# Kernel tuning notes

Measured on AMD Instinct MI355X. Metric: run time of the kernel, lower is better.

The kernel has to match this reference:

```python
import jax, jax.numpy as jnp
import numpy as np

EMBED_DIM = 1024
NUM_HEADS = 16
MICRO_HEADS = 8
HEAD_DIM = EMBED_DIM // NUM_HEADS
N_BLOCKS = NUM_HEADS // MICRO_HEADS
B, N = 2, 2048


def setup_inputs() -> dict:
    key = jax.random.key(0)
    ks = jax.random.split(key, 9)
    s = 1.0 / np.sqrt(EMBED_DIM)
    return {
        "x": jax.random.normal(ks[0], (B, N, EMBED_DIM), dtype=jnp.float32),
        "Wq": jax.random.uniform(ks[1], (EMBED_DIM, EMBED_DIM), jnp.float32, -s, s),
        "bq": jax.random.uniform(ks[2], (EMBED_DIM,), jnp.float32, -s, s),
        "Wk": jax.random.uniform(ks[3], (EMBED_DIM, EMBED_DIM), jnp.float32, -s, s),
        "bk": jax.random.uniform(ks[4], (EMBED_DIM,), jnp.float32, -s, s),
        "Wv": jax.random.uniform(ks[5], (EMBED_DIM, EMBED_DIM), jnp.float32, -s, s),
        "bv": jax.random.uniform(ks[6], (EMBED_DIM,), jnp.float32, -s, s),
        "Wo": jax.random.uniform(ks[7], (EMBED_DIM, EMBED_DIM), jnp.float32, -s, s),
        "bo": jax.random.uniform(ks[8], (EMBED_DIM,), jnp.float32, -s, s),
    }


def _scramble(t, b, n):
    # Replicates torch's Qh[:, :, hs:he, :].contiguous().view(B*mh, N, dh)
    # which is a raw row-major reshape mixing (N, mh) -> (mh, N) per batch.
    # (B, N, E) -> (B, N, nb, mh, dh) -> (B, nb, N, mh, dh) -> raw reshape -> (B, nb, mh, N, dh)
    t = t.reshape(b, n, N_BLOCKS, MICRO_HEADS, HEAD_DIM)
    t = jnp.transpose(t, (0, 2, 1, 3, 4))
    return t.reshape(b, N_BLOCKS, MICRO_HEADS, n, HEAD_DIM)


def reference(x, Wq, bq, Wk, bk, Wv, bv, Wo, bo):
    b, n, e = x.shape
    scale = HEAD_DIM ** -0.5
    Q = x @ Wq.T + bq
    K = x @ Wk.T + bk
    V = x @ Wv.T + bv
    q = _scramble(Q, b, n)  # (B, nb, mh, N, dh)
    k = _scramble(K, b, n)
    v = _scramble(V, b, n)
    s = jnp.einsum("bgmqd,bgmkd->bgmqk", q, k) * scale  # (B, nb, mh, N, N)
    causal = jnp.tril(jnp.ones((n, n), dtype=bool))
    s = jnp.where(causal, s, -jnp.inf)
    p = jax.nn.softmax(s, axis=-1)
    ctx = jnp.einsum("bgmqk,bgmkd->bgmqd", p, v)  # (B, nb, mh, N, dh)
    # inverse raw reshape: (mh, N, dh) -> (N, mh*dh) per (b, g), then concat blocks
    ctx = ctx.reshape(b, N_BLOCKS, n, MICRO_HEADS * HEAD_DIM)
    ctx = jnp.transpose(ctx, (0, 2, 1, 3)).reshape(b, n, e)
    return ctx @ Wo.T + bo
```

## Files before the change

### kernel.cpp

```cpp
#include <hip/hip_runtime.h>
#include <hip/hip_bf16.h>


typedef unsigned short ushortT;
typedef __attribute__((ext_vector_type(8))) short short8;
typedef __attribute__((ext_vector_type(4))) float floatx4;
typedef __attribute__((ext_vector_type(2))) unsigned int uintx2;

__device__ inline void gl_lds16(const ushortT* g, ushortT* lds) {
    __builtin_amdgcn_global_load_lds(
        (const __attribute__((address_space(1))) unsigned int*)g,
        (__attribute__((address_space(3))) unsigned int*)lds, 16, 0, 0);
}

__global__ __launch_bounds__(256) void cvt_bf16(
    const float* __restrict__ x,
    const float* __restrict__ Wq, const float* __restrict__ Wk,
    const float* __restrict__ Wv, const float* __restrict__ Wo,
    ushortT* __restrict__ xb, ushortT* __restrict__ Wb)
{
    const unsigned tid = blockIdx.x * 256 + threadIdx.x;
    const size_t e = (size_t)tid * 8;
    const float* src;
    ushortT* dst;
    size_t off;
    if (e < (size_t)(4u << 20)) { src = x; dst = xb; off = e; }
    else {
        const size_t r = e - (size_t)(4u << 20);
        const int wsel = (int)(r >> 20);
        off = r & 0xFFFFFu;
        src = (wsel == 0) ? Wq : (wsel == 1) ? Wk : (wsel == 2) ? Wv : Wo;
        dst = Wb + ((size_t)wsel << 20);
    }
    const float4 f0 = ((const float4*)(src + off))[0];
    const float4 f1 = ((const float4*)(src + off))[1];
    union { __hip_bfloat162 h[4]; uint4 u; } pk;
    pk.h[0] = __float22bfloat162_rn(float2{f0.x, f0.y});
    pk.h[1] = __float22bfloat162_rn(float2{f0.z, f0.w});
    pk.h[2] = __float22bfloat162_rn(float2{f1.x, f1.y});
    pk.h[3] = __float22bfloat162_rn(float2{f1.z, f1.w});
    *(uint4*)(dst + off) = pk.u;
}

__global__ __launch_bounds__(512, 2) void gemm_qkv_8p(
    const ushortT* __restrict__ A, const ushortT* __restrict__ Wst,
    const float* __restrict__ b0, const float* __restrict__ b1, const float* __restrict__ b2,
    ushortT* __restrict__ O0, ushortT* __restrict__ O1, ushortT* __restrict__ O2)
{
    __shared__ __align__(16) ushortT sm[65536];

    const int t = threadIdx.x;
    const int bid = blockIdx.x;
    const int wg = (bid & 7) * 24 + (bid >> 3);
    const int mt = wg / 12;
    const int nt = wg - mt * 12;
    const int m0 = mt * 256;
    const int mat = nt >> 2;
    const int n0 = (nt & 3) * 256;
    const ushortT* W = Wst + ((size_t)mat << 20);
    const float* bias = (mat == 0) ? b0 : (mat == 1) ? b1 : b2;
    ushortT* Out     = (mat == 0) ? O0 : (mat == 1) ? O1 : O2;
    const float oscale = (mat == 0) ? 0.18033688f : 1.0f;

    const int w = t >> 6, lane = t & 63;
    const int wm = w >> 2, wn = w & 3;
    const int col16 = lane & 15, quad = lane >> 4;
    const int c7 = col16 & 7;

    const int ko[2] = { ((0 + quad) ^ c7) << 3, ((4 + quad) ^ c7) << 3 };
    const int xbase = (wm * 128 + col16) * 64;
    const int wbase = (wn * 64 + col16) * 64;

    const int trow = t >> 3;
    const int sch = (t & 7) ^ (trow & 7);
    const ushortT* gA[4]; const ushortT* gB[4];
    #pragma unroll
    for (int q = 0; q < 4; q++) {
        gA[q] = A + (size_t)(m0 + q * 64 + trow) * 1024 + sch * 8;
        gB[q] = W + (size_t)(n0 + q * 64 + trow) * 1024 + sch * 8;
    }
    const int dst0 = (w << 6) * 8;

    floatx4 acc[8][4];
    #pragma unroll
    for (int i = 0; i < 8; i++)
        #pragma unroll
        for (int j = 0; j < 4; j++) acc[i][j] = (floatx4)0.0f;

    auto issue8 = [&](const int ab, const int bb) {
        #pragma unroll
        for (int q = 0; q < 4; q++) {
            gl_lds16(gA[q], sm + ab + dst0 + q * 4096);
            gl_lds16(gB[q], sm + bb + dst0 + q * 4096);
            gA[q] += 64; gB[q] += 64;
        }
    };

    auto group = [&](const int ab, const int bb) {
        short8 bw[4];
        #pragma unroll
        for (int ks = 0; ks < 2; ks++) {
            #pragma unroll
            for (int mh = 0; mh < 2; mh++) {
                short8 bx[4];
                if (mh == 0) {
                    #pragma unroll
                    for (int nf = 0; nf < 4; nf++)
                        bw[nf] = *(const short8*)(sm + bb + wbase + nf * 1024 + ko[ks]);
                }
                #pragma unroll
                for (int j = 0; j < 4; j++)
                    bx[j] = *(const short8*)(sm + ab + xbase + (mh * 4 + j) * 1024 + ko[ks]);
                __builtin_amdgcn_s_barrier();
                __builtin_amdgcn_s_setprio(1);
                #pragma unroll
                for (int j = 0; j < 4; j++)
                    #pragma unroll
                    for (int nf = 0; nf < 4; nf++)
                        acc[mh * 4 + j][nf] = __builtin_amdgcn_mfma_f32_16x16x32_bf16(
                            bw[nf], bx[j], acc[mh * 4 + j][nf], 0, 0, 0);
                __builtin_amdgcn_s_setprio(0);
                __builtin_amdgcn_s_barrier();
            }
        }
    };

    issue8(0, 16384);
    issue8(32768, 49152);

    #pragma unroll 1
    for (int it = 0; it < 7; ++it) {
        asm volatile("s_waitcnt vmcnt(8)" ::: "memory");
        __builtin_amdgcn_s_barrier();
        group(0, 16384);
        issue8(0, 16384);
        asm volatile("s_waitcnt vmcnt(8)" ::: "memory");
        __builtin_amdgcn_s_barrier();
        group(32768, 49152);
        issue8(32768, 49152);
    }
    asm volatile("s_waitcnt vmcnt(8)" ::: "memory");
    __builtin_amdgcn_s_barrier();
    group(0, 16384);
    asm volatile("s_waitcnt vmcnt(0)" ::: "memory");
    __builtin_amdgcn_s_barrier();
    group(32768, 49152);

    #pragma unroll
    for (int mf = 0; mf < 8; mf++) {
        const int m = m0 + wm * 128 + mf * 16 + col16;
        #pragma unroll
        for (int nf = 0; nf < 4; nf++) {
            const int nb = n0 + wn * 64 + nf * 16 + quad * 4;
            const float4 bv4 = *(const float4*)(bias + nb);
            const float v0 = (acc[mf][nf][0] + bv4.x) * oscale;
            const float v1 = (acc[mf][nf][1] + bv4.y) * oscale;
            const float v2 = (acc[mf][nf][2] + bv4.z) * oscale;
            const float v3 = (acc[mf][nf][3] + bv4.w) * oscale;
            union { __hip_bfloat162 h[2]; unsigned long long u; } pk2;
            pk2.h[0] = __float22bfloat162_rn(float2{v0, v1});
            pk2.h[1] = __float22bfloat162_rn(float2{v2, v3});
            *(unsigned long long*)(Out + (size_t)m * 1024 + nb) = pk2.u;
        }
    }
}

template <bool OUT_F32, bool N64>
__global__ __launch_bounds__(256) void gemm_lds(
    const ushortT* __restrict__ A, const ushortT* __restrict__ Wst,
    const float* __restrict__ b0, const float* __restrict__ b1, const float* __restrict__ b2,
    void* __restrict__ O0, void* __restrict__ O1, void* __restrict__ O2)
{
    constexpr int NT = N64 ? 64 : 128;
    constexpr int NJ = N64 ? 2 : 4;
    constexpr int WQ = N64 ? 2 : 4;
    __shared__ __align__(16) ushortT As[128 * 64];
    __shared__ __align__(16) ushortT Bs[NT * 64];
    const int t = threadIdx.x;
    const int m0 = blockIdx.y * 128;
    const int n0g = blockIdx.x * NT;
    const int mat = n0g >> 10;
    const int n0 = n0g & 1023;
    const ushortT* W = Wst + ((size_t)mat << 20);
    const float* bias = (mat == 0) ? b0 : (mat == 1) ? b1 : b2;
    void* Out        = (mat == 0) ? O0 : (mat == 1) ? O1 : O2;

    const int w = t >> 6, lane = t & 63;
    const int wm = w >> 1, wn = w & 1;
    const int col16 = lane & 15, quad = lane >> 4;

    floatx4 acc[4][NJ];
    for (int i = 0; i < 4; i++)
        for (int j = 0; j < NJ; j++) acc[i][j] = (floatx4)0.0f;

    const int cid0 = w * (N64 ? 128 : 256) + lane;

    for (int k0 = 0; k0 < 1024; k0 += 64) {
        #pragma unroll
        for (int q = 0; q < 4; q++) {
            const int cid = w * 256 + q * 64 + lane;
            const int row = cid >> 3;
            const int sch = (cid & 7) ^ (row & 7);
            gl_lds16(A + (size_t)(m0 + row) * 1024 + k0 + sch * 8,
                     As + (size_t)(w * 256 + q * 64) * 8);
        }
        #pragma unroll
        for (int q = 0; q < WQ; q++) {
            const int cid = cid0 + q * 64;
            const int row = cid >> 3;
            const int sch = (cid & 7) ^ (row & 7);
            gl_lds16(W + (size_t)(n0 + row) * 1024 + k0 + sch * 8,
                     Bs + (size_t)(w * (N64 ? 128 : 256) + q * 64) * 8);
        }
        __syncthreads();
        #pragma unroll
        for (int ks = 0; ks < 64; ks += 32) {
            const int cbase = (ks >> 3) + quad;
            const int sw = col16 & 7;
            short8 a[4], b[NJ];
            #pragma unroll
            for (int i = 0; i < 4; i++) {
                const int row = wm * 64 + i * 16 + col16;
                a[i] = *(const short8*)(As + row * 64 + ((cbase ^ sw) << 3));
            }
            #pragma unroll
            for (int j = 0; j < NJ; j++) {
                const int row = wn * (NT / 2) + j * 16 + col16;
                b[j] = *(const short8*)(Bs + row * 64 + ((cbase ^ sw) << 3));
            }
            #pragma unroll
            for (int i = 0; i < 4; i++)
                #pragma unroll
                for (int j = 0; j < NJ; j++)
                    acc[i][j] = __builtin_amdgcn_mfma_f32_16x16x32_bf16(b[j], a[i], acc[i][j], 0, 0, 0);
        }
        __syncthreads();
    }

    #pragma unroll
    for (int i = 0; i < 4; i++) {
        const int m = m0 + wm * 64 + i * 16 + col16;
        #pragma unroll
        for (int j = 0; j < NJ; j++) {
            const int nb = n0 + wn * (NT / 2) + j * 16 + quad * 4;
            const float4 bv4 = *(const float4*)(bias + nb);
            const float v0 = acc[i][j][0] + bv4.x;
            const float v1 = acc[i][j][1] + bv4.y;
            const float v2 = acc[i][j][2] + bv4.z;
            const float v3 = acc[i][j][3] + bv4.w;
            if constexpr (OUT_F32) {
                *(float4*)((float*)Out + (size_t)m * 1024 + nb) = float4{v0, v1, v2, v3};
            } else {
                union { __hip_bfloat162 h[2]; unsigned long long u; } pk2;
                pk2.h[0] = __float22bfloat162_rn(float2{v0, v1});
                pk2.h[1] = __float22bfloat162_rn(float2{v2, v3});
                *(unsigned long long*)((ushortT*)Out + (size_t)m * 1024 + nb) = pk2.u;
            }
        }
    }
}

__global__ __launch_bounds__(256) void transpose_v(
    const ushortT* __restrict__ Vb, ushortT* __restrict__ VT)
{
    __shared__ ushortT L[64 * 65];
    const int bid = blockIdx.x;
    const int pt = bid & 31, s = bid >> 5;
    const int bb = s >> 4, g = (s >> 3) & 1, mh = s & 7;
    const size_t baseoff = (size_t)bb * 2048 * 1024 + (size_t)g * 512;
    const int t = threadIdx.x;
    {
        const int pr = t >> 2, seg = t & 3;
        const int i = mh * 2048 + pt * 64 + pr;
        const uint4* src = (const uint4*)(Vb + baseoff + (size_t)(i >> 3) * 1024 + (i & 7) * 64 + seg * 16);
        union { uint4 u[2]; ushortT h[16]; } tmp;
        tmp.u[0] = src[0]; tmp.u[1] = src[1];
        #pragma unroll
        for (int d = 0; d < 16; d++) L[pr * 65 + seg * 16 + d] = tmp.h[d];
    }
    __syncthreads();
    {
        const int dc = t >> 2, pseg = t & 3;
        union { uint4 u[2]; ushortT h[16]; } tmp;
        #pragma unroll
        for (int j = 0; j < 16; j++) tmp.h[j] = L[(pseg * 16 + j) * 65 + dc];
        uint4* dst = (uint4*)(VT + (size_t)s * 64 * 2048 + (size_t)dc * 2048 + pt * 64 + pseg * 16);
        dst[0] = tmp.u[0]; dst[1] = tmp.u[1];
    }
}

__global__ __launch_bounds__(256) void attn(
    const ushortT* __restrict__ Qb, const ushortT* __restrict__ Kb,
    const ushortT* __restrict__ VT, ushortT* __restrict__ Cb)
{
    __shared__ __align__(16) ushortT lds[16384];

    const int t = threadIdx.x;
    const int bid = blockIdx.x;
    const int xcd = bid & 7;
    const int u = bid >> 3;
    const int s = xcd * 4 + (u & 3);
    const int x5 = u >> 2;
    const int qt = (x5 < 8) ? x5 : (x5 < 16) ? (39 - x5)
                 : (x5 < 24) ? (x5 - 8) : (47 - x5);
    const int bb = s >> 4, g = (s >> 3) & 1, mh = s & 7;

    const int w = t >> 6, lane = t & 63;
    const int col16 = lane & 15, quad = lane >> 4;

    const size_t baseoff = (size_t)bb * 2048 * 1024 + (size_t)g * 512;
    const size_t vtbase  = (size_t)s * 64 * 2048;
    const int i0 = mh * 2048 + qt * 64;
    const int qloc = w * 16 + col16;
    const int c7 = col16 & 7;

    short8 qreg[2];
    {
        const int i = i0 + qloc;
        const ushortT* p = Qb + baseoff + (size_t)(i >> 3) * 1024 + (i & 7) * 64;
        qreg[0] = *(const short8*)(p + quad * 8);
        qreg[1] = *(const short8*)(p + 32 + quad * 8);
    }

    int kbo[2];
    kbo[0] = col16 * 64 + (((0 + quad) ^ c7) << 3);
    kbo[1] = col16 * 64 + (((4 + quad) ^ c7) << 3);

    const int cid0 = w * 128 + lane, cid1 = cid0 + 64;
    const int row0 = cid0 >> 3, sch0 = (cid0 & 7) ^ (row0 & 7);
    const int row1 = cid1 >> 3, sch1 = (cid1 & 7) ^ (row1 & 7);
    const int jr0 = mh * 2048 + row0;
    const int jr1 = mh * 2048 + row1;
    const ushortT* gk0 = Kb + baseoff + (size_t)(jr0 >> 3) * 1024 + (jr0 & 7) * 64 + sch0 * 8;
    const ushortT* gk1 = Kb + baseoff + (size_t)(jr1 >> 3) * 1024 + (jr1 & 7) * 64 + sch1 * 8;
    const ushortT* gv0 = VT + vtbase + (size_t)row0 * 2048 + sch0 * 8;
    const ushortT* gv1 = VT + vtbase + (size_t)row1 * 2048 + sch1 * 8;
    const int sdK = w * 1024;

    auto stage = [&](int sb) {
        gl_lds16(gk0, lds + sb + sdK);
        gl_lds16(gk1, lds + sb + sdK + 512);
        gl_lds16(gv0, lds + sb + 8192 + sdK);
        gl_lds16(gv1, lds + sb + 8192 + sdK + 512);
        gk0 += 8192; gk1 += 8192; gv0 += 64; gv1 += 64;
    };

    float l4[4] = {0.f, 0.f, 0.f, 0.f};
    floatx4 Oacc[4];
    for (int c = 0; c < 4; c++) Oacc[c] = (floatx4)0.0f;

    stage(0);
    int sb = 4096;
    for (int kt = 0; kt <= qt; ++kt) {
        __syncthreads();
        if (kt < qt) { stage(sb); sb ^= 4096; }

        floatx4 sc[4];
        for (int c = 0; c < 4; c++) sc[c] = (floatx4)0.0f;
        #pragma unroll
        for (int h = 0; h < 2; h++) {
            const short8 bq = qreg[h];
            #pragma unroll
            for (int c = 0; c < 4; c++) {
                const short8 ak = *(const short8*)(lds + kbo[h] + c * 1024);
                sc[c] = __builtin_amdgcn_mfma_f32_16x16x32_bf16(ak, bq, sc[c], 0, 0, 0);
            }
        }

        if (kt == qt) {
            #pragma unroll
            for (int c = 0; c < 4; c++)
                #pragma unroll
                for (int r = 0; r < 4; r++)
                    if ((c * 16 + quad * 4 + r) > qloc) sc[c][r] = -1e30f;
        }

        unsigned pw[4][2];
        #pragma unroll
        for (int c = 0; c < 4; c++) {
            float pv0 = __builtin_amdgcn_exp2f(sc[c][0]);
            float pv1 = __builtin_amdgcn_exp2f(sc[c][1]);
            float pv2 = __builtin_amdgcn_exp2f(sc[c][2]);
            float pv3 = __builtin_amdgcn_exp2f(sc[c][3]);
            l4[0] += pv0; l4[1] += pv1; l4[2] += pv2; l4[3] += pv3;
            union { __hip_bfloat162 h; unsigned u; } a, b;
            a.h = __float22bfloat162_rn(float2{pv0, pv1});
            b.h = __float22bfloat162_rn(float2{pv2, pv3});
            pw[c][0] = a.u; pw[c][1] = b.u;
        }

        #pragma unroll
        for (int h = 0; h < 2; h++) {
            unsigned dw[4];
            #pragma unroll
            for (int uu = 0; uu < 2; uu++) {
                uintx2 s32 = __builtin_amdgcn_permlane32_swap(pw[2 * h][uu], pw[2 * h + 1][uu], false, false);
                uintx2 s16 = __builtin_amdgcn_permlane16_swap(s32.x, s32.y, false, false);
                dw[uu] = s16.x; dw[2 + uu] = s16.y;
            }
            union { unsigned u[4]; short8 s; } bpu;
            bpu.u[0] = dw[0]; bpu.u[1] = dw[1]; bpu.u[2] = dw[2]; bpu.u[3] = dw[3];
            const short8 bp = bpu.s;
            #pragma unroll
            for (int c = 0; c < 4; c++) {
                const short8 av = *(const short8*)(lds + kbo[h] + 8192 + c * 1024);
                Oacc[c] = __builtin_amdgcn_mfma_f32_16x16x32_bf16(av, bp, Oacc[c], 0, 0, 0);
            }
        }

        kbo[0] ^= 4096; kbo[1] ^= 4096;
    }

    float l_s = (l4[0] + l4[1]) + (l4[2] + l4[3]);
    l_s += __shfl_xor(l_s, 16);
    l_s += __shfl_xor(l_s, 32);

    {
        const int i = i0 + qloc;
        const float inv = 1.0f / l_s;
        ushortT* dst = Cb + baseoff + (size_t)(i >> 3) * 1024 + (i & 7) * 64;
        #pragma unroll
        for (int c = 0; c < 4; c++) {
            union { __hip_bfloat162 h[2]; unsigned long long u; } pk2;
            pk2.h[0] = __float22bfloat162_rn(float2{Oacc[c][0] * inv, Oacc[c][1] * inv});
            pk2.h[1] = __float22bfloat162_rn(float2{Oacc[c][2] * inv, Oacc[c][3] * inv});
            *(unsigned long long*)(dst + c * 16 + quad * 4) = pk2.u;
        }
    }
}

extern "C" void kernel_launch(void* const* d_in, const int* in_sizes, int n_in,
                              void* d_out, int out_size, void* d_ws, size_t ws_size,
                              hipStream_t stream)
{
    const float* x  = (const float*)d_in[0];
    const float* Wq = (const float*)d_in[1];
    const float* bq = (const float*)d_in[2];
    const float* Wk = (const float*)d_in[3];
    const float* bk = (const float*)d_in[4];
    const float* Wv = (const float*)d_in[5];
    const float* bv = (const float*)d_in[6];
    const float* Wo = (const float*)d_in[7];
    const float* bo = (const float*)d_in[8];

    const size_t M1 = (size_t)1024 * 1024;
    ushortT* Wb  = (ushortT*)d_ws;
    ushortT* xb  = Wb + 4 * M1;
    ushortT* Qb  = xb + 4 * M1;
    ushortT* Kb  = Qb + 4 * M1;
    ushortT* Vb  = (ushortT*)d_out;
    ushortT* VTb = xb;
    ushortT* Cb  = Qb;

    dim3 blk(256);
    cvt_bf16<<<dim3(4096), blk, 0, stream>>>(x, Wq, Wk, Wv, Wo, xb, Wb);
    gemm_qkv_8p<<<dim3(192), dim3(512), 0, stream>>>(
        xb, Wb, bq, bk, bv, Qb, Kb, Vb);
    transpose_v<<<dim3(1024), blk, 0, stream>>>(Vb, VTb);
    attn<<<dim3(1024), blk, 0, stream>>>(Qb, Kb, VTb, Cb);
    gemm_lds<true, true><<<dim3(16, 32), blk, 0, stream>>>(
        Cb, Wb + 3 * M1, bo, bo, bo, d_out, d_out, d_out);
}
```

Measured before the change: 184.0 us.

## Double query tile per attention block to reuse K/V LDS tiles

Each attention block now handles 128 query rows instead of 64, with each wave owning two 16-row query fragments that share the same K and V LDS reads. The grid halves to 512 blocks and the causal tile schedule is remapped to pair tiles for load balance. This cuts K/V global loads and LDS reads per query, at the cost of more registers per thread (doubled accumulators and scores), fewer blocks in flight, and extra masked work on the diagonal tiles.

```diff
diff --git a/kernel.cpp b/kernel.cpp
--- a/kernel.cpp
+++ b/kernel.cpp
@@ -300,9 +300,8 @@
     const int xcd = bid & 7;
     const int u = bid >> 3;
     const int s = xcd * 4 + (u & 3);
-    const int x5 = u >> 2;
-    const int qt = (x5 < 8) ? x5 : (x5 < 16) ? (39 - x5)
-                 : (x5 < 24) ? (x5 - 8) : (47 - x5);
+    const int x4 = u >> 2;
+    const int p = (x4 < 8) ? x4 : 23 - x4;
     const int bb = s >> 4, g = (s >> 3) & 1, mh = s & 7;
 
     const int w = t >> 6, lane = t & 63;
@@ -310,16 +309,19 @@
 
     const size_t baseoff = (size_t)bb * 2048 * 1024 + (size_t)g * 512;
     const size_t vtbase  = (size_t)s * 64 * 2048;
-    const int i0 = mh * 2048 + qt * 64;
-    const int qloc = w * 16 + col16;
+    const int i0 = mh * 2048 + p * 128;
+    const int ntile = 2 * p + 2;
     const int c7 = col16 & 7;
 
-    short8 qreg[2];
-    {
-        const int i = i0 + qloc;
-        const ushortT* p = Qb + baseoff + (size_t)(i >> 3) * 1024 + (i & 7) * 64;
-        qreg[0] = *(const short8*)(p + quad * 8);
-        qreg[1] = *(const short8*)(p + 32 + quad * 8);
+    const int qloc[2] = { w * 32 + col16, w * 32 + 16 + col16 };
+
+    short8 qreg[2][2];
+    #pragma unroll
+    for (int qf = 0; qf < 2; qf++) {
+        const int i = i0 + qloc[qf];
+        const ushortT* ptr = Qb + baseoff + (size_t)(i >> 3) * 1024 + (i & 7) * 64;
+        qreg[qf][0] = *(const short8*)(ptr + quad * 8);
+        qreg[qf][1] = *(const short8*)(ptr + 32 + quad * 8);
     }
 
     int kbo[2];
@@ -345,85 +347,111 @@
         gk0 += 8192; gk1 += 8192; gv0 += 64; gv1 += 64;
     };
 
-    float l4[4] = {0.f, 0.f, 0.f, 0.f};
-    floatx4 Oacc[4];
-    for (int c = 0; c < 4; c++) Oacc[c] = (floatx4)0.0f;
+    float l4[2][4];
+    floatx4 Oacc[2][4];
+    #pragma unroll
+    for (int qf = 0; qf < 2; qf++)
+        #pragma unroll
+        for (int c = 0; c < 4; c++) { Oacc[qf][c] = (floatx4)0.0f; l4[qf][c] = 0.f; }
 
     stage(0);
     int sb = 4096;
-    for (int kt = 0; kt <= qt; ++kt) {
+    #pragma unroll 1
+    for (int kt = 0; kt < ntile; ++kt) {
         __syncthreads();
-        if (kt < qt) { stage(sb); sb ^= 4096; }
-
-        floatx4 sc[4];
-        for (int c = 0; c < 4; c++) sc[c] = (floatx4)0.0f;
+        if (kt < ntile - 1) { stage(sb); sb ^= 4096; }
+
+        floatx4 sc[2][4];
+        #pragma unroll
+        for (int qf = 0; qf < 2; qf++)
+            #pragma unroll
+            for (int c = 0; c < 4; c++) sc[qf][c] = (floatx4)0.0f;
         #pragma unroll
         for (int h = 0; h < 2; h++) {
-            const short8 bq = qreg[h];
+            short8 ak[4];
+            #pragma unroll
+            for (int c = 0; c < 4; c++)
+                ak[c] = *(const short8*)(lds + kbo[h] + c * 1024);
+            #pragma unroll
+            for (int qf = 0; qf < 2; qf++)
+                #pragma unroll
+                for (int c = 0; c < 4; c++)
+                    sc[qf][c] = __builtin_amdgcn_mfma_f32_16x16x32_bf16(
+                        ak[c], qreg[qf][h], sc[qf][c], 0, 0, 0);
+        }
+
+        const int dk = kt - 2 * p;
+        if (dk >= 0) {
+            #pragma unroll
+            for (int qf = 0; qf < 2; qf++) {
+                const int qe = qloc[qf] - 64 * dk;
+                #pragma unroll
+                for (int c = 0; c < 4; c++)
+                    #pragma unroll
+                    for (int r = 0; r < 4; r++)
+                        if ((c * 16 + quad * 4 + r) > qe) sc[qf][c][r] = -1e30f;
+            }
+        }
+
+        unsigned pw[2][4][2];
+        #pragma unroll
+        for (int qf = 0; qf < 2; qf++)
             #pragma unroll
             for (int c = 0; c < 4; c++) {
-                const short8 ak = *(const short8*)(lds + kbo[h] + c * 1024);
-                sc[c] = __builtin_amdgcn_mfma_f32_16x16x32_bf16(ak, bq, sc[c], 0, 0, 0);
-            }
-        }
-
-        if (kt == qt) {
+                float pv0 = __builtin_amdgcn_exp2f(sc[qf][c][0]);
+                float pv1 = __builtin_amdgcn_exp2f(sc[qf][c][1]);
+                float pv2 = __builtin_amdgcn_exp2f(sc[qf][c][2]);
+                float pv3 = __builtin_amdgcn_exp2f(sc[qf][c][3]);
+                l4[qf][0] += pv0; l4[qf][1] += pv1;
+                l4[qf][2] += pv2; l4[qf][3] += pv3;
+                union { __hip_bfloat162 h; unsigned u; } a, b;
+                a.h = __float22bfloat162_rn(float2{pv0, pv1});
+                b.h = __float22bfloat162_rn(float2{pv2, pv3});
+                pw[qf][c][0] = a.u; pw[qf][c][1] = b.u;
+            }
+
+        #pragma unroll
+        for (int h = 0; h < 2; h++) {
+            short8 av[4];
             #pragma unroll
             for (int c = 0; c < 4; c++)
-                #pragma unroll
-                for (int r = 0; r < 4; r++)
-                    if ((c * 16 + quad * 4 + r) > qloc) sc[c][r] = -1e30f;
-        }
-
-        unsigned pw[4][2];
-        #pragma unroll
-        for (int c = 0; c < 4; c++) {
-            float pv0 = __builtin_amdgcn_exp2f(sc[c][0]);
-            float pv1 = __builtin_amdgcn_exp2f(sc[c][1]);
-            float pv2 = __builtin_amdgcn_exp2f(sc[c][2]);
-            float pv3 = __builtin_amdgcn_exp2f(sc[c][3]);
-            l4[0] += pv0; l4[1] += pv1; l4[2] += pv2; l4[3] += pv3;
-            union { __hip_bfloat162 h; unsigned u; } a, b;
-            a.h = __float22bfloat162_rn(float2{pv0, pv1});
-            b.h = __float22bfloat162_rn(float2{pv2, pv3});
-            pw[c][0] = a.u; pw[c][1] = b.u;
-        }
-
-        #pragma unroll
-        for (int h = 0; h < 2; h++) {
-            unsigned dw[4];
-            #pragma unroll
-            for (int uu = 0; uu < 2; uu++) {
-                uintx2 s32 = __builtin_amdgcn_permlane32_swap(pw[2 * h][uu], pw[2 * h + 1][uu], false, false);
-                uintx2 s16 = __builtin_amdgcn_permlane16_swap(s32.x, s32.y, false, false);
-                dw[uu] = s16.x; dw[2 + uu] = s16.y;
-            }
-            union { unsigned u[4]; short8 s; } bpu;
-            bpu.u[0] = dw[0]; bpu.u[1] = dw[1]; bpu.u[2] = dw[2]; bpu.u[3] = dw[3];
-            const short8 bp = bpu.s;
-            #pragma unroll
-            for (int c = 0; c < 4; c++) {
-                const short8 av = *(const short8*)(lds + kbo[h] + 8192 + c * 1024);
-                Oacc[c] = __builtin_amdgcn_mfma_f32_16x16x32_bf16(av, bp, Oacc[c], 0, 0, 0);
+                av[c] = *(const short8*)(lds + kbo[h] + 8192 + c * 1024);
+            #pragma unroll
+            for (int qf = 0; qf < 2; qf++) {
+                unsigned dw[4];
+                #pragma unroll
+                for (int uu = 0; uu < 2; uu++) {
+                    uintx2 s32 = __builtin_amdgcn_permlane32_swap(
+                        pw[qf][2 * h][uu], pw[qf][2 * h + 1][uu], false, false);
+                    uintx2 s16 = __builtin_amdgcn_permlane16_swap(s32.x, s32.y, false, false);
+                    dw[uu] = s16.x; dw[2 + uu] = s16.y;
+                }
+                union { unsigned u[4]; short8 s; } bpu;
+                bpu.u[0] = dw[0]; bpu.u[1] = dw[1]; bpu.u[2] = dw[2]; bpu.u[3] = dw[3];
+                const short8 bp = bpu.s;
+                #pragma unroll
+                for (int c = 0; c < 4; c++)
+                    Oacc[qf][c] = __builtin_amdgcn_mfma_f32_16x16x32_bf16(
+                        av[c], bp, Oacc[qf][c], 0, 0, 0);
             }
         }
 
         kbo[0] ^= 4096; kbo[1] ^= 4096;
     }
 
-    float l_s = (l4[0] + l4[1]) + (l4[2] + l4[3]);
-    l_s += __shfl_xor(l_s, 16);
-    l_s += __shfl_xor(l_s, 32);
-
-    {
-        const int i = i0 + qloc;
+    #pragma unroll
+    for (int qf = 0; qf < 2; qf++) {
+        float l_s = (l4[qf][0] + l4[qf][1]) + (l4[qf][2] + l4[qf][3]);
+        l_s += __shfl_xor(l_s, 16);
+        l_s += __shfl_xor(l_s, 32);
         const float inv = 1.0f / l_s;
+        const int i = i0 + qloc[qf];
         ushortT* dst = Cb + baseoff + (size_t)(i >> 3) * 1024 + (i & 7) * 64;
         #pragma unroll
         for (int c = 0; c < 4; c++) {
             union { __hip_bfloat162 h[2]; unsigned long long u; } pk2;
-            pk2.h[0] = __float22bfloat162_rn(float2{Oacc[c][0] * inv, Oacc[c][1] * inv});
-            pk2.h[1] = __float22bfloat162_rn(float2{Oacc[c][2] * inv, Oacc[c][3] * inv});
+            pk2.h[0] = __float22bfloat162_rn(float2{Oacc[qf][c][0] * inv, Oacc[qf][c][1] * inv});
+            pk2.h[1] = __float22bfloat162_rn(float2{Oacc[qf][c][2] * inv, Oacc[qf][c][3] * inv});
             *(unsigned long long*)(dst + c * 16 + quad * 4) = pk2.u;
         }
     }
@@ -457,7 +485,7 @@
     gemm_qkv_8p<<<dim3(192), dim3(512), 0, stream>>>(
         xb, Wb, bq, bk, bv, Qb, Kb, Vb);
     transpose_v<<<dim3(1024), blk, 0, stream>>>(Vb, VTb);
-    attn<<<dim3(1024), blk, 0, stream>>>(Qb, Kb, VTb, Cb);
+    attn<<<dim3(512), blk, 0, stream>>>(Qb, Kb, VTb, Cb);
     gemm_lds<true, true><<<dim3(16, 32), blk, 0, stream>>>(
         Cb, Wb + 3 * M1, bo, bo, bo, d_out, d_out, d_out);
 }
```

Result: slower. 189.0 us (+2.8%).

## Switch attention to 32x32x16 MFMA with two-wave blocks of 32 query rows

Applied to the files above, without the earlier changes.

Rewrites the attention kernel to use 32x32x16 bf16 MFMA tiles instead of 16x16x32, with 128-thread blocks where each wave handles 32 query rows of the 64-row tile. The P-matrix repacking uses only permlane32 swaps, the causal mask and output layout are remapped for the 32x32 accumulator layout, and s_setprio is raised around the MFMA bursts. The intent is fewer MFMA issues, fewer LDS reads per FLOP and less shuffle overhead. The trade-off is more registers per wave and half as many waves per block, which may lower occupancy and latency hiding.

```diff
diff --git a/kernel.cpp b/kernel.cpp
--- a/kernel.cpp
+++ b/kernel.cpp
@@ -5,6 +5,7 @@
 typedef unsigned short ushortT;
 typedef __attribute__((ext_vector_type(8))) short short8;
 typedef __attribute__((ext_vector_type(4))) float floatx4;
+typedef __attribute__((ext_vector_type(16))) float floatx16;
 typedef __attribute__((ext_vector_type(2))) unsigned int uintx2;
 
 __device__ inline void gl_lds16(const ushortT* g, ushortT* lds) {
@@ -289,7 +290,7 @@
     }
 }
 
-__global__ __launch_bounds__(256) void attn(
+__global__ __launch_bounds__(128) void attn(
     const ushortT* __restrict__ Qb, const ushortT* __restrict__ Kb,
     const ushortT* __restrict__ VT, ushortT* __restrict__ Cb)
 {
@@ -306,126 +307,142 @@
     const int bb = s >> 4, g = (s >> 3) & 1, mh = s & 7;
 
     const int w = t >> 6, lane = t & 63;
-    const int col16 = lane & 15, quad = lane >> 4;
+    const int l31 = lane & 31, h = lane >> 5;
 
     const size_t baseoff = (size_t)bb * 2048 * 1024 + (size_t)g * 512;
     const size_t vtbase  = (size_t)s * 64 * 2048;
     const int i0 = mh * 2048 + qt * 64;
-    const int qloc = w * 16 + col16;
-    const int c7 = col16 & 7;
-
-    short8 qreg[2];
+    const int qloc = w * 32 + l31;
+
+    short8 qreg[4];
     {
         const int i = i0 + qloc;
         const ushortT* p = Qb + baseoff + (size_t)(i >> 3) * 1024 + (i & 7) * 64;
-        qreg[0] = *(const short8*)(p + quad * 8);
-        qreg[1] = *(const short8*)(p + 32 + quad * 8);
-    }
-
-    int kbo[2];
-    kbo[0] = col16 * 64 + (((0 + quad) ^ c7) << 3);
-    kbo[1] = col16 * 64 + (((4 + quad) ^ c7) << 3);
-
-    const int cid0 = w * 128 + lane, cid1 = cid0 + 64;
-    const int row0 = cid0 >> 3, sch0 = (cid0 & 7) ^ (row0 & 7);
-    const int row1 = cid1 >> 3, sch1 = (cid1 & 7) ^ (row1 & 7);
-    const int jr0 = mh * 2048 + row0;
-    const int jr1 = mh * 2048 + row1;
-    const ushortT* gk0 = Kb + baseoff + (size_t)(jr0 >> 3) * 1024 + (jr0 & 7) * 64 + sch0 * 8;
-    const ushortT* gk1 = Kb + baseoff + (size_t)(jr1 >> 3) * 1024 + (jr1 & 7) * 64 + sch1 * 8;
-    const ushortT* gv0 = VT + vtbase + (size_t)row0 * 2048 + sch0 * 8;
-    const ushortT* gv1 = VT + vtbase + (size_t)row1 * 2048 + sch1 * 8;
-    const int sdK = w * 1024;
-
-    auto stage = [&](int sb) {
-        gl_lds16(gk0, lds + sb + sdK);
-        gl_lds16(gk1, lds + sb + sdK + 512);
-        gl_lds16(gv0, lds + sb + 8192 + sdK);
-        gl_lds16(gv1, lds + sb + 8192 + sdK + 512);
-        gk0 += 8192; gk1 += 8192; gv0 += 64; gv1 += 64;
+        #pragma unroll
+        for (int dc = 0; dc < 4; dc++)
+            qreg[dc] = *(const short8*)(p + dc * 16 + h * 8);
+    }
+
+    int off[2][4];
+    #pragma unroll
+    for (int a = 0; a < 2; a++)
+        #pragma unroll
+        for (int b = 0; b < 4; b++)
+            off[a][b] = (a * 32 + l31) * 64 + ((((b << 1) + h) ^ (lane & 7)) << 3);
+
+    const ushortT* gk[4]; const ushortT* gv[4];
+    int ldk[4];
+    #pragma unroll
+    for (int j = 0; j < 4; j++) {
+        const int cid = j * 128 + t;
+        const int row = cid >> 3;
+        const int sch = (cid & 7) ^ (row & 7);
+        const int jr = mh * 2048 + row;
+        gk[j] = Kb + baseoff + (size_t)(jr >> 3) * 1024 + (jr & 7) * 64 + sch * 8;
+        gv[j] = VT + vtbase + (size_t)row * 2048 + sch * 8;
+        ldk[j] = j * 1024 + w * 512;
+    }
+
+    auto stage = [&](int sbw) {
+        #pragma unroll
+        for (int j = 0; j < 4; j++) {
+            gl_lds16(gk[j], lds + sbw + ldk[j]);
+            gl_lds16(gv[j], lds + sbw + 8192 + ldk[j]);
+            gk[j] += 8192; gv[j] += 64;
+        }
     };
 
     float l4[4] = {0.f, 0.f, 0.f, 0.f};
-    floatx4 Oacc[4];
-    for (int c = 0; c < 4; c++) Oacc[c] = (floatx4)0.0f;
+    floatx16 Oacc[2];
+    Oacc[0] = (floatx16)0.0f; Oacc[1] = (floatx16)0.0f;
 
     stage(0);
     int sb = 4096;
+    int sbR = 0;
+    #pragma unroll 1
     for (int kt = 0; kt <= qt; ++kt) {
         __syncthreads();
         if (kt < qt) { stage(sb); sb ^= 4096; }
 
-        floatx4 sc[4];
-        for (int c = 0; c < 4; c++) sc[c] = (floatx4)0.0f;
-        #pragma unroll
-        for (int h = 0; h < 2; h++) {
-            const short8 bq = qreg[h];
-            #pragma unroll
-            for (int c = 0; c < 4; c++) {
-                const short8 ak = *(const short8*)(lds + kbo[h] + c * 1024);
-                sc[c] = __builtin_amdgcn_mfma_f32_16x16x32_bf16(ak, bq, sc[c], 0, 0, 0);
-            }
-        }
+        floatx16 sc[2];
+        sc[0] = (floatx16)0.0f; sc[1] = (floatx16)0.0f;
+        __builtin_amdgcn_s_setprio(1);
+        #pragma unroll
+        for (int dc = 0; dc < 4; dc++) {
+            #pragma unroll
+            for (int a = 0; a < 2; a++) {
+                const short8 ak = *(const short8*)(lds + sbR + off[a][dc]);
+                sc[a] = __builtin_amdgcn_mfma_f32_32x32x16_bf16(ak, qreg[dc], sc[a], 0, 0, 0);
+            }
+        }
+        __builtin_amdgcn_s_setprio(0);
 
         if (kt == qt) {
             #pragma unroll
-            for (int c = 0; c < 4; c++)
+            for (int a = 0; a < 2; a++)
                 #pragma unroll
-                for (int r = 0; r < 4; r++)
-                    if ((c * 16 + quad * 4 + r) > qloc) sc[c][r] = -1e30f;
-        }
-
-        unsigned pw[4][2];
-        #pragma unroll
-        for (int c = 0; c < 4; c++) {
-            float pv0 = __builtin_amdgcn_exp2f(sc[c][0]);
-            float pv1 = __builtin_amdgcn_exp2f(sc[c][1]);
-            float pv2 = __builtin_amdgcn_exp2f(sc[c][2]);
-            float pv3 = __builtin_amdgcn_exp2f(sc[c][3]);
-            l4[0] += pv0; l4[1] += pv1; l4[2] += pv2; l4[3] += pv3;
-            union { __hip_bfloat162 h; unsigned u; } a, b;
-            a.h = __float22bfloat162_rn(float2{pv0, pv1});
-            b.h = __float22bfloat162_rn(float2{pv2, pv3});
-            pw[c][0] = a.u; pw[c][1] = b.u;
-        }
-
-        #pragma unroll
-        for (int h = 0; h < 2; h++) {
-            unsigned dw[4];
-            #pragma unroll
-            for (int uu = 0; uu < 2; uu++) {
-                uintx2 s32 = __builtin_amdgcn_permlane32_swap(pw[2 * h][uu], pw[2 * h + 1][uu], false, false);
-                uintx2 s16 = __builtin_amdgcn_permlane16_swap(s32.x, s32.y, false, false);
-                dw[uu] = s16.x; dw[2 + uu] = s16.y;
-            }
-            union { unsigned u[4]; short8 s; } bpu;
-            bpu.u[0] = dw[0]; bpu.u[1] = dw[1]; bpu.u[2] = dw[2]; bpu.u[3] = dw[3];
-            const short8 bp = bpu.s;
-            #pragma unroll
-            for (int c = 0; c < 4; c++) {
-                const short8 av = *(const short8*)(lds + kbo[h] + 8192 + c * 1024);
-                Oacc[c] = __builtin_amdgcn_mfma_f32_16x16x32_bf16(av, bp, Oacc[c], 0, 0, 0);
-            }
-        }
-
-        kbo[0] ^= 4096; kbo[1] ^= 4096;
+                for (int r = 0; r < 16; r++) {
+                    const int key = a * 32 + (r & 3) + ((r >> 2) << 3) + 4 * h;
+                    if (key > qloc) sc[a][r] = -1e30f;
+                }
+        }
+
+        unsigned sp[2][8];
+        #pragma unroll
+        for (int a = 0; a < 2; a++)
+            #pragma unroll
+            for (int i2 = 0; i2 < 8; i2++) {
+                const float p0 = __builtin_amdgcn_exp2f(sc[a][2 * i2]);
+                const float p1 = __builtin_amdgcn_exp2f(sc[a][2 * i2 + 1]);
+                l4[(2 * i2) & 3] += p0;
+                l4[(2 * i2 + 1) & 3] += p1;
+                union { __hip_bfloat162 hh; unsigned uu; } pk;
+                pk.hh = __float22bfloat162_rn(float2{p0, p1});
+                sp[a][i2] = pk.uu;
+            }
+
+        #pragma unroll
+        for (int a = 0; a < 2; a++) {
+            #pragma unroll
+            for (int kc = 0; kc < 2; kc++) {
+                const uintx2 s0 = __builtin_amdgcn_permlane32_swap(
+                    sp[a][4 * kc + 0], sp[a][4 * kc + 2], false, false);
+                const uintx2 s1 = __builtin_amdgcn_permlane32_swap(
+                    sp[a][4 * kc + 1], sp[a][4 * kc + 3], false, false);
+                union { unsigned uu[4]; short8 ss; } bp;
+                bp.uu[0] = s0.x; bp.uu[1] = s1.x; bp.uu[2] = s0.y; bp.uu[3] = s1.y;
+                const int kcg = a * 2 + kc;
+                __builtin_amdgcn_s_setprio(1);
+                #pragma unroll
+                for (int dt = 0; dt < 2; dt++) {
+                    const short8 av = *(const short8*)(lds + sbR + 8192 + off[dt][kcg]);
+                    Oacc[dt] = __builtin_amdgcn_mfma_f32_32x32x16_bf16(av, bp.ss, Oacc[dt], 0, 0, 0);
+                }
+                __builtin_amdgcn_s_setprio(0);
+            }
+        }
+
+        sbR ^= 4096;
     }
 
     float l_s = (l4[0] + l4[1]) + (l4[2] + l4[3]);
-    l_s += __shfl_xor(l_s, 16);
     l_s += __shfl_xor(l_s, 32);
+    const float inv = 1.0f / l_s;
 
     {
         const int i = i0 + qloc;
-        const float inv = 1.0f / l_s;
         ushortT* dst = Cb + baseoff + (size_t)(i >> 3) * 1024 + (i & 7) * 64;
         #pragma unroll
-        for (int c = 0; c < 4; c++) {
-            union { __hip_bfloat162 h[2]; unsigned long long u; } pk2;
-            pk2.h[0] = __float22bfloat162_rn(float2{Oacc[c][0] * inv, Oacc[c][1] * inv});
-            pk2.h[1] = __float22bfloat162_rn(float2{Oacc[c][2] * inv, Oacc[c][3] * inv});
-            *(unsigned long long*)(dst + c * 16 + quad * 4) = pk2.u;
-        }
+        for (int dt = 0; dt < 2; dt++)
+            #pragma unroll
+            for (int rq = 0; rq < 4; rq++) {
+                union { __hip_bfloat162 hh[2]; unsigned long long uu; } pk2;
+                pk2.hh[0] = __float22bfloat162_rn(
+                    float2{Oacc[dt][4 * rq + 0] * inv, Oacc[dt][4 * rq + 1] * inv});
+                pk2.hh[1] = __float22bfloat162_rn(
+                    float2{Oacc[dt][4 * rq + 2] * inv, Oacc[dt][4 * rq + 3] * inv});
+                *(unsigned long long*)(dst + dt * 32 + 8 * rq + 4 * h) = pk2.uu;
+            }
     }
 }
 
@@ -457,7 +474,7 @@
     gemm_qkv_8p<<<dim3(192), dim3(512), 0, stream>>>(
         xb, Wb, bq, bk, bv, Qb, Kb, Vb);
     transpose_v<<<dim3(1024), blk, 0, stream>>>(Vb, VTb);
-    attn<<<dim3(1024), blk, 0, stream>>>(Qb, Kb, VTb, Cb);
+    attn<<<dim3(1024), dim3(128), 0, stream>>>(Qb, Kb, VTb, Cb);
     gemm_lds<true, true><<<dim3(16, 32), blk, 0, stream>>>(
         Cb, Wb + 3 * M1, bo, bo, bo, d_out, d_out, d_out);
 }
```

Measured after the change: 190.9 us. +3.8%, slower.

## Restructure QKV GEMM into 4-stage K=32 LDS pipeline

Applied to the files above, without the earlier changes.

Replaces the double-buffered K=64 tile pipeline in the fused QKV GEMM with a 4-slot ring of K=32 tiles, keeping three loads in flight ahead of compute. The LDS layout and XOR swizzle change to 32-element rows, and the global-to-LDS copy is re-partitioned so each thread issues 4 loads per stage. The goal is deeper prefetch to hide global latency. In exchange there are more loop iterations and barriers per unit of K, and the vmcnt accounting becomes harder to get right.

```diff
diff --git a/kernel.cpp b/kernel.cpp
--- a/kernel.cpp
+++ b/kernel.cpp
@@ -42,7 +42,7 @@
     *(uint4*)(dst + off) = pk.u;
 }
 
-__global__ __launch_bounds__(512, 2) void gemm_qkv_8p(
+__global__ __launch_bounds__(512, 2) void gemm_qkv_d4(
     const ushortT* __restrict__ A, const ushortT* __restrict__ Wst,
     const float* __restrict__ b0, const float* __restrict__ b1, const float* __restrict__ b2,
     ushortT* __restrict__ O0, ushortT* __restrict__ O1, ushortT* __restrict__ O2)
@@ -65,21 +65,24 @@
     const int w = t >> 6, lane = t & 63;
     const int wm = w >> 2, wn = w & 3;
     const int col16 = lane & 15, quad = lane >> 4;
-    const int c7 = col16 & 7;
-
-    const int ko[2] = { ((0 + quad) ^ c7) << 3, ((4 + quad) ^ c7) << 3 };
-    const int xbase = (wm * 128 + col16) * 64;
-    const int wbase = (wn * 64 + col16) * 64;
-
-    const int trow = t >> 3;
-    const int sch = (t & 7) ^ (trow & 7);
-    const ushortT* gA[4]; const ushortT* gB[4];
-    #pragma unroll
-    for (int q = 0; q < 4; q++) {
-        gA[q] = A + (size_t)(m0 + q * 64 + trow) * 1024 + sch * 8;
-        gB[q] = W + (size_t)(n0 + q * 64 + trow) * 1024 + sch * 8;
-    }
-    const int dst0 = (w << 6) * 8;
+
+    const int ko = (quad ^ (col16 & 3)) << 3;
+    int xoff[8], woff[4];
+    #pragma unroll
+    for (int i = 0; i < 8; i++) xoff[i] = (wm * 128 + i * 16 + col16) * 32 + ko;
+    #pragma unroll
+    for (int nf = 0; nf < 4; nf++) woff[nf] = (wn * 64 + nf * 16 + col16) * 32 + ko;
+
+    const ushortT* gA[2]; const ushortT* gB[2];
+    #pragma unroll
+    for (int q = 0; q < 2; q++) {
+        const int cid = q * 512 + t;
+        const int row = cid >> 2;
+        const int sch = (cid & 3) ^ (row & 3);
+        gA[q] = A + (size_t)(m0 + row) * 1024 + sch * 8;
+        gB[q] = W + (size_t)(n0 + row) * 1024 + sch * 8;
+    }
+    const int dstw = w * 512;
 
     floatx4 acc[8][4];
     #pragma unroll
@@ -87,64 +90,65 @@
         #pragma unroll
         for (int j = 0; j < 4; j++) acc[i][j] = (floatx4)0.0f;
 
-    auto issue8 = [&](const int ab, const int bb) {
-        #pragma unroll
-        for (int q = 0; q < 4; q++) {
-            gl_lds16(gA[q], sm + ab + dst0 + q * 4096);
-            gl_lds16(gB[q], sm + bb + dst0 + q * 4096);
-            gA[q] += 64; gB[q] += 64;
+    auto issue4 = [&](const int slot) {
+        #pragma unroll
+        for (int q = 0; q < 2; q++) {
+            gl_lds16(gA[q], sm + slot + q * 4096 + dstw);
+            gl_lds16(gB[q], sm + slot + 8192 + q * 4096 + dstw);
+            gA[q] += 32; gB[q] += 32;
         }
     };
 
-    auto group = [&](const int ab, const int bb) {
-        short8 bw[4];
-        #pragma unroll
-        for (int ks = 0; ks < 2; ks++) {
-            #pragma unroll
-            for (int mh = 0; mh < 2; mh++) {
-                short8 bx[4];
-                if (mh == 0) {
-                    #pragma unroll
-                    for (int nf = 0; nf < 4; nf++)
-                        bw[nf] = *(const short8*)(sm + bb + wbase + nf * 1024 + ko[ks]);
-                }
-                #pragma unroll
-                for (int j = 0; j < 4; j++)
-                    bx[j] = *(const short8*)(sm + ab + xbase + (mh * 4 + j) * 1024 + ko[ks]);
-                __builtin_amdgcn_s_barrier();
-                __builtin_amdgcn_s_setprio(1);
-                #pragma unroll
-                for (int j = 0; j < 4; j++)
-                    #pragma unroll
-                    for (int nf = 0; nf < 4; nf++)
-                        acc[mh * 4 + j][nf] = __builtin_amdgcn_mfma_f32_16x16x32_bf16(
-                            bw[nf], bx[j], acc[mh * 4 + j][nf], 0, 0, 0);
-                __builtin_amdgcn_s_setprio(0);
-                __builtin_amdgcn_s_barrier();
-            }
-        }
+    auto group = [&](const int slot) {
+        short8 bw[4], bx[4];
+        #pragma unroll
+        for (int nf = 0; nf < 4; nf++)
+            bw[nf] = *(const short8*)(sm + slot + 8192 + woff[nf]);
+        #pragma unroll
+        for (int j = 0; j < 4; j++)
+            bx[j] = *(const short8*)(sm + slot + xoff[j]);
+        __builtin_amdgcn_s_barrier();
+        __builtin_amdgcn_s_setprio(1);
+        #pragma unroll
+        for (int j = 0; j < 4; j++)
+            #pragma unroll
+            for (int nf = 0; nf < 4; nf++)
+                acc[j][nf] = __builtin_amdgcn_mfma_f32_16x16x32_bf16(
+                    bw[nf], bx[j], acc[j][nf], 0, 0, 0);
+        __builtin_amdgcn_s_setprio(0);
+        __builtin_amdgcn_s_barrier();
+        #pragma unroll
+        for (int j = 0; j < 4; j++)
+            bx[j] = *(const short8*)(sm + slot + xoff[4 + j]);
+        __builtin_amdgcn_s_barrier();
+        __builtin_amdgcn_s_setprio(1);
+        #pragma unroll
+        for (int j = 0; j < 4; j++)
+            #pragma unroll
+            for (int nf = 0; nf < 4; nf++)
+                acc[4 + j][nf] = __builtin_amdgcn_mfma_f32_16x16x32_bf16(
+                    bw[nf], bx[j], acc[4 + j][nf], 0, 0, 0);
+        __builtin_amdgcn_s_setprio(0);
+        __builtin_amdgcn_s_barrier();
     };
 
-    issue8(0, 16384);
-    issue8(32768, 49152);
+    issue4(0 * 16384);
+    issue4(1 * 16384);
+    issue4(2 * 16384);
 
     #pragma unroll 1
-    for (int it = 0; it < 7; ++it) {
+    for (int tt = 0; tt < 30; ++tt) {
         asm volatile("s_waitcnt vmcnt(8)" ::: "memory");
         __builtin_amdgcn_s_barrier();
-        group(0, 16384);
-        issue8(0, 16384);
-        asm volatile("s_waitcnt vmcnt(8)" ::: "memory");
-        __builtin_amdgcn_s_barrier();
-        group(32768, 49152);
-        issue8(32768, 49152);
-    }
-    asm volatile("s_waitcnt vmcnt(8)" ::: "memory");
+        group((tt & 3) * 16384);
+        if (tt < 29) issue4(((tt + 3) & 3) * 16384);
+    }
+    asm volatile("s_waitcnt vmcnt(4)" ::: "memory");
     __builtin_amdgcn_s_barrier();
-    group(0, 16384);
+    group(2 * 16384);
     asm volatile("s_waitcnt vmcnt(0)" ::: "memory");
     __builtin_amdgcn_s_barrier();
-    group(32768, 49152);
+    group(3 * 16384);
 
     #pragma unroll
     for (int mf = 0; mf < 8; mf++) {
@@ -454,7 +458,7 @@
 
     dim3 blk(256);
     cvt_bf16<<<dim3(4096), blk, 0, stream>>>(x, Wq, Wk, Wv, Wo, xb, Wb);
-    gemm_qkv_8p<<<dim3(192), dim3(512), 0, stream>>>(
+    gemm_qkv_d4<<<dim3(192), dim3(512), 0, stream>>>(
         xb, Wb, bq, bk, bv, Qb, Kb, Vb);
     transpose_v<<<dim3(1024), blk, 0, stream>>>(Vb, VTb);
     attn<<<dim3(1024), blk, 0, stream>>>(Qb, Kb, VTb, Cb);
```

Result: no change. 184.8 us (+0.4%).
